# Kernel tuning notes

Measured on AMD Instinct MI355X. Metric: run time of the kernel, lower is better.

## Reference

```python
import jax, jax.numpy as jnp
import numpy as np

B = 64          # batch
N = 256         # input_dim (number of MPS sites / pixels)
BOND = 128      # bond dimension
DF = 2          # feature dimension per pixel
OUT = 10        # output classes
EPS = 1e-12


def _xavier_uniform(key, shape, fan_in, fan_out, gain):
    bound = gain * np.sqrt(6.0 / (fan_in + fan_out))
    return jax.random.uniform(key, shape, jnp.float32, -bound, bound)


def setup_inputs() -> dict:
    key = jax.random.key(0)
    k_x, k_c0, k_cr, k_cl = jax.random.split(key, 4)
    gain = float(np.sqrt(2.0 / (1.0 + 0.01 ** 2)))  # leaky_relu gain
    x = jax.random.uniform(k_x, (B, N), dtype=jnp.float32)  # pixels in [0,1]
    # core 0: (1, DF, BOND); torch fan_in = DF*BOND, fan_out = 1*BOND
    core0 = _xavier_uniform(k_c0, (1, DF, BOND), DF * BOND, BOND, gain)
    # remaining N-1 cores: (BOND, DF, BOND); fan_in = DF*BOND, fan_out = BOND*BOND... torch: fan_in = shape[1]*shape[2] = DF*BOND, fan_out = shape[0]*shape[2] = BOND*BOND? No: fan_out = shape[0]*prod(shape[2:]) = BOND*BOND
    cores = _xavier_uniform(k_cr, (N - 1, BOND, DF, BOND), DF * BOND, BOND * BOND, gain)
    classifier = _xavier_uniform(k_cl, (OUT, BOND), BOND, OUT, gain)
    return {"x": x, "core0": core0, "cores": cores, "classifier": classifier}


def _mps_forward(x, core0, cores, classifier):
    b = x.shape[0]
    H = core0.shape[-1]
    # feature map: pixel v -> (1-v, v)
    feats = jnp.stack([1.0 - x, x], axis=-1)                  # (B, N, DF)
    # contract each core with its pixel feature
    special = jnp.einsum('ldh,bd->blh', core0, feats[:, 0])   # (B, 1, H)
    others = jnp.einsum('nldh,bnd->bnlh', cores, feats[:, 1:])  # (B, N-1, H, H)
    log_norm = jnp.zeros((b,), dtype=x.dtype)

    # log-depth tree contraction; loop bound is static (trace-time)
    while 1 + others.shape[1] > 1:
        # pad the special (1,H) leftmost tensor up to (H,H) with zero rows
        padded = jnp.pad(special, ((0, 0), (0, H - special.shape[1]), (0, 0)))
        full = jnp.concatenate([padded[:, None], others], axis=1)  # (B, K, H, H)
        K = full.shape[1]
        odd = (K % 2 != 0)
        if odd:
            last = full[:, -1]
            full = full[:, :-1]
        s1 = full[:, 0::2]                                    # (B, P, H, H)
        s2 = full[:, 1::2]
        cp = jnp.matmul(s1, s2)                               # (B, P, H, H)
        norms = jnp.maximum(
            jnp.sqrt(jnp.sum(cp * cp, axis=(-2, -1))), EPS)   # (B, P)
        log_norm = log_norm + jnp.sum(jnp.log(norms), axis=1)
        cp = cp / norms[:, :, None, None]
        special = cp[:, 0, 0:1, :]                            # keep only row 0
        others = cp[:, 1:]
        if odd:
            others = jnp.concatenate([others, last[:, None]], axis=1)

    mps_out = special[:, 0, :]                                # (B, H)
    logits = mps_out @ classifier.T + log_norm[:, None]      # (B, OUT)
    return logits


def reference(x, core0, cores, classifier):
    return _mps_forward(x, core0, cores, classifier)
```

## Files before the change

### kernel.cpp

```cpp
#include <hip/hip_runtime.h>
#include <stdint.h>


typedef unsigned short u16;
typedef __attribute__((ext_vector_type(8))) short short8;
typedef __attribute__((ext_vector_type(4))) float f32x4;

#define HP 136

__device__ __forceinline__ u16 f2b(float f) {
  uint32_t u = __builtin_bit_cast(uint32_t, f);
  u += 0x7FFFu + ((u >> 16) & 1u);
  return (u16)(u >> 16);
}
__device__ __forceinline__ float b2f(u16 b) {
  uint32_t u = ((uint32_t)b) << 16;
  return __builtin_bit_cast(float, u);
}

struct AccW { f32x4 t[2][2]; };

__device__ __forceinline__ void mfma_w16(const u16* Alds, const u16* Blds,
                                         AccW& acc) {
  const int tid = threadIdx.x;
  const int wid = tid >> 6, lane = tid & 63;
  const int wm = (wid >> 2) * 32, wn = (wid & 3) * 32;
  const int l16 = lane & 15, quad = lane >> 4;
#pragma unroll
  for (int tm = 0; tm < 2; tm++)
#pragma unroll
    for (int tn = 0; tn < 2; tn++)
      acc.t[tm][tn] = (f32x4){0.f, 0.f, 0.f, 0.f};
#pragma unroll
  for (int kk = 0; kk < 128; kk += 32) {
    short8 af[2], bf[2];
#pragma unroll
    for (int t = 0; t < 2; t++) {
      af[t] = *(const short8*)(Alds + (wm + t * 16 + l16) * HP + kk + quad * 8);
      bf[t] = *(const short8*)(Blds + (wn + t * 16 + l16) * HP + kk + quad * 8);
    }
#pragma unroll
    for (int tm = 0; tm < 2; tm++)
#pragma unroll
      for (int tn = 0; tn < 2; tn++)
        acc.t[tm][tn] = __builtin_amdgcn_mfma_f32_16x16x32_bf16(
            af[tm], bf[tn], acc.t[tm][tn], 0, 0, 0);
  }
}

__device__ __forceinline__ float acc_sumsq(const AccW& acc) {
  float ss = 0.f;
#pragma unroll
  for (int tm = 0; tm < 2; tm++)
#pragma unroll
    for (int tn = 0; tn < 2; tn++)
#pragma unroll
      for (int i = 0; i < 4; i++) {
        float v = acc.t[tm][tn][i];
        ss += v * v;
      }
  return ss;
}

__device__ __forceinline__ void bounce_store(u16* Lb, const AccW& acc, float scale,
                                             bool transposed) {
  const int tid = threadIdx.x;
  const int wid = tid >> 6, lane = tid & 63;
  const int wm = (wid >> 2) * 32, wn = (wid & 3) * 32;
  const int l16 = lane & 15, quad = lane >> 4;
#pragma unroll
  for (int tm = 0; tm < 2; tm++)
#pragma unroll
    for (int tn = 0; tn < 2; tn++)
#pragma unroll
      for (int i = 0; i < 4; i++) {
        int r = wm + tm * 16 + quad * 4 + i;
        int c = wn + tn * 16 + l16;
        int key = transposed ? c : r, sec = transposed ? r : c;
        Lb[key * HP + sec] = f2b(acc.t[tm][tn][i] * scale);
      }
}

__device__ __forceinline__ void copy_out(const u16* Lb, u16* out) {
  const int tid = threadIdx.x;
#pragma unroll
  for (int i = 0; i < 2; i++) {
    int g8 = tid + i * 1024;
    int row = g8 >> 4, c8 = g8 & 15;
    *(uint4*)(out + g8 * 8) = *(const uint4*)(Lb + row * HP + c8 * 8);
  }
}

__device__ __forceinline__ float block_sum(float v, float* red, int nw) {
#pragma unroll
  for (int off = 32; off > 0; off >>= 1) v += __shfl_down(v, off);
  int wid = threadIdx.x >> 6;
  if ((threadIdx.x & 63) == 0) red[wid] = v;
  __syncthreads();
  if (threadIdx.x == 0) {
    float s = 0.f;
    for (int w = 0; w < nw; w++) s += red[w];
    red[0] = s;
  }
  __syncthreads();
  float s = red[0];
  __syncthreads();
  return s;
}

__global__ __launch_bounds__(1024) void k1(const float* __restrict__ cores,
                                           u16* __restrict__ T) {
  __shared__ u16 Ald[128 * HP], B0[128 * HP], B1[128 * HP];
  const int j = blockIdx.x;
  const int p = blockIdx.y;
  const float* c1 = cores + (size_t)(2 * j + 1) * 32768;
  const float* c2 = cores + (size_t)(2 * j + 2) * 32768;
  const int tid = threadIdx.x;
#pragma unroll 4
  for (int i = 0; i < 16; i++) {
    int lh = tid + i * 1024;
    int l = lh >> 7, h = lh & 127;
    float a0 = c1[(l * 2 + 0) * 128 + h];
    float av = p ? (c1[(l * 2 + 1) * 128 + h] - a0) : a0;
    Ald[l * HP + h] = f2b(av);
    float b0 = c2[(l * 2 + 0) * 128 + h];
    float b1 = c2[(l * 2 + 1) * 128 + h];
    B0[h * HP + l] = f2b(b0);
    B1[h * HP + l] = f2b(b1 - b0);
  }
  __syncthreads();
  const bool tr = (j % 2) == 0;
  u16* Tj = T + ((size_t)j * 4 + p * 2) * 16384;
  AccW q0, q1;
  mfma_w16(Ald, B0, q0);
  mfma_w16(Ald, B1, q1);
  __syncthreads();
  bounce_store(Ald, q0, 1.f, tr); __syncthreads();
  copy_out(Ald, Tj + 0 * 16384);  __syncthreads();
  bounce_store(Ald, q1, 1.f, tr); __syncthreads();
  copy_out(Ald, Tj + 1 * 16384);
}

__global__ __launch_bounds__(1024, 8) void k1b(const u16* __restrict__ T,
                                               u16* __restrict__ TT) {
  __shared__ u16 Ald[128 * HP], Bld[128 * HP];
  const int t = blockIdx.x;
  const int j2 = blockIdx.y;
  const int m1 = 2 * j2 + 1, m2 = 2 * j2 + 2;
  const u16* TA = T + ((size_t)m1 * 4 + (t >> 2)) * 16384;
  const u16* TB = T + ((size_t)m2 * 4 + (t & 3)) * 16384;
  const int tid = threadIdx.x;
#pragma unroll
  for (int i = 0; i < 2; i++) {
    int g8 = tid + i * 1024;
    int r = g8 >> 4, c8 = g8 & 15;
    *(uint4*)(Ald + r * HP + c8 * 8) = *(const uint4*)(TA + g8 * 8);
    *(uint4*)(Bld + r * HP + c8 * 8) = *(const uint4*)(TB + g8 * 8);
  }
  __syncthreads();
  AccW acc;
  mfma_w16(Ald, Bld, acc);
  __syncthreads();
  bounce_store(Ald, acc, 1.f, (j2 % 2) == 0);
  __syncthreads();
  copy_out(Ald, TT + ((size_t)j2 * 16 + t) * 16384);
}

__global__ __launch_bounds__(256) void k1c(const u16* __restrict__ TT,
                                           float* __restrict__ Gpart) {
  __shared__ float Gp[1024];
  const int j2 = blockIdx.x, kc = blockIdx.y;
  const int tid = threadIdx.x;
  const int w = tid >> 6, lane = tid & 63;
  const int l16 = lane & 15, quad = lane >> 4;
  const u16* V = TT + (size_t)j2 * 16 * 16384 + (size_t)l16 * 16384;
  const int k0 = kc * 4096 + w * 1024;
  f32x4 acc = (f32x4){0.f, 0.f, 0.f, 0.f};
  for (int kk = k0; kk < k0 + 1024; kk += 32) {
    short8 av = *(const short8*)(V + kk + quad * 8);
    acc = __builtin_amdgcn_mfma_f32_16x16x32_bf16(av, av, acc, 0, 0, 0);
  }
#pragma unroll
  for (int i = 0; i < 4; i++)
    Gp[w * 256 + (quad * 4 + i) * 16 + l16] = acc[i];
  __syncthreads();
  Gpart[((size_t)j2 * 4 + kc) * 256 + tid] =
      Gp[tid] + Gp[256 + tid] + Gp[512 + tid] + Gp[768 + tid];
}

__global__ __launch_bounds__(128) void k2ns(const float* __restrict__ x,
                                            const float* __restrict__ Gpart,
                                            const float* __restrict__ core0,
                                            const float* __restrict__ cores,
                                            const u16* __restrict__ T,
                                            float* __restrict__ cbuf,
                                            float* __restrict__ sA,
                                            float* __restrict__ logs) {
  __shared__ float Gs[256];
  __shared__ float svec[128];
  __shared__ float red[8];
  const int bx = blockIdx.x, tid = threadIdx.x;
  if (bx < 63) {
    const int j2 = bx;
#pragma unroll
    for (int i = 0; i < 2; i++) {
      int t2 = tid + i * 128;
      float s = 0.f;
#pragma unroll
      for (int kc = 0; kc < 4; kc++)
        s += Gpart[((size_t)j2 * 4 + kc) * 256 + t2];
      Gs[t2] = s;
    }
    __syncthreads();
    if (tid < 64) {
      const int b = tid;
      const float* xb = x + b * 256;
      const int m1 = 2 * j2 + 1, m2 = 2 * j2 + 2;
      float a1 = xb[2 * m1 + 2], b1 = xb[2 * m1 + 3];
      float a2 = xb[2 * m2 + 2], b2 = xb[2 * m2 + 3];
      float c1[4] = {1.f, b1, a1, a1 * b1};
      float c2[4] = {1.f, b2, a2, a2 * b2};
      float c[16];
#pragma unroll
      for (int p = 0; p < 4; p++)
#pragma unroll
        for (int q = 0; q < 4; q++) c[p * 4 + q] = c1[p] * c2[q];
      float n2 = 0.f;
#pragma unroll
      for (int t = 0; t < 16; t++) {
        float s = 0.f;
#pragma unroll
        for (int u = 0; u < 16; u++) s += Gs[t * 16 + u] * c[u];
        n2 += c[t] * s;
      }
      float n = fmaxf(sqrtf(n2), 1e-12f);
      logs[b * 127 + 1 + j2] = logf(n);
      float inv = 1.f / n;
#pragma unroll
      for (int t = 0; t < 16; t++)
        cbuf[((size_t)j2 * 64 + b) * 16 + t] = c[t] * inv;
    }
  } else {
    const int b = bx - 63;
    const float* xb = x + b * 256;
    float x0 = xb[0], x1 = xb[1];
    svec[tid] = core0[tid] * (1.f - x0) + core0[128 + tid] * x0;
    __syncthreads();
    float acc1 = 0.f;
    for (int k = 0; k < 128; k++) {
      float m0 = cores[(k * 2 + 0) * 128 + tid];
      float m1 = cores[(k * 2 + 1) * 128 + tid];
      acc1 += svec[k] * (m0 + x1 * (m1 - m0));
    }
    float tot = block_sum(acc1 * acc1, red, 2);
    float n1 = fmaxf(sqrtf(tot), 1e-12f);
    float ln = logf(n1);
    svec[tid] = acc1 / n1;
    __syncthreads();
    float a = xb[2], bb = xb[3], ab = a * bb;
    float acc2 = 0.f;
    for (int k8 = 0; k8 < 16; k8++) {
      union { uint4 v; u16 s[8]; } q00, q01, q10, q11;
      q00.v = *(const uint4*)(T + tid * 128 + k8 * 8);
      q01.v = *(const uint4*)(T + 16384 + tid * 128 + k8 * 8);
      q10.v = *(const uint4*)(T + 32768 + tid * 128 + k8 * 8);
      q11.v = *(const uint4*)(T + 49152 + tid * 128 + k8 * 8);
#pragma unroll
      for (int e = 0; e < 8; e++) {
        float pk = b2f(q00.s[e]) + a * b2f(q10.s[e]) + bb * b2f(q01.s[e]) +
                   ab * b2f(q11.s[e]);
        acc2 += svec[k8 * 8 + e] * pk;
      }
    }
    float tot2 = block_sum(acc2 * acc2, red, 2);
    float n2 = fmaxf(sqrtf(tot2), 1e-12f);
    sA[b * 128 + tid] = acc2 / n2;
    if (tid == 0) logs[b * 127 + 0] = ln + logf(n2);
  }
}

__global__ __launch_bounds__(256, 4) void k2c(const u16* __restrict__ TT,
                                              const float* __restrict__ cbuf,
                                              u16* __restrict__ M0) {
  const int slice = blockIdx.x;
  const int j2 = blockIdx.y;
  const int tid = threadIdx.x;
  const int e0 = slice * 512 + tid * 2;
  float v[16][2];
#pragma unroll
  for (int t = 0; t < 16; t++) {
    union { uint32_t u; u16 s[2]; } q;
    q.u = *(const uint32_t*)(TT + ((size_t)j2 * 16 + t) * 16384 + e0);
    v[t][0] = b2f(q.s[0]);
    v[t][1] = b2f(q.s[1]);
  }
  const float4* cb4 = (const float4*)(cbuf + (size_t)j2 * 1024);
  u16* out = M0 + (size_t)j2 * 16384 + e0;
#pragma unroll 4
  for (int b = 0; b < 64; b++) {
    float4 c0 = cb4[b * 4 + 0];
    float4 c1 = cb4[b * 4 + 1];
    float4 c2 = cb4[b * 4 + 2];
    float4 c3 = cb4[b * 4 + 3];
    float cc[16] = {c0.x, c0.y, c0.z, c0.w, c1.x, c1.y, c1.z, c1.w,
                    c2.x, c2.y, c2.z, c2.w, c3.x, c3.y, c3.z, c3.w};
    float o0 = 0.f, o1 = 0.f;
#pragma unroll
    for (int t = 0; t < 16; t++) {
      o0 += cc[t] * v[t][0];
      o1 += cc[t] * v[t][1];
    }
    union { uint32_t u; u16 s[2]; } r;
    r.s[0] = f2b(o0);
    r.s[1] = f2b(o1);
    *(uint32_t*)(out + (size_t)b * 63 * 16384) = r.u;
  }
}

__global__ __launch_bounds__(1024, 8) void roundk(const u16* __restrict__ In,
                                                  u16* __restrict__ Out,
                                                  const float* __restrict__ sIn,
                                                  float* __restrict__ sOut,
                                                  float* __restrict__ logs,
                                                  int count_in, int slot0) {
  __shared__ u16 Ald[128 * HP], Bld[128 * HP];
  __shared__ float red[16];
  const int b = blockIdx.y, p = blockIdx.x, tid = threadIdx.x;

  if (p == 0) {
    float* svec = (float*)Ald;
    if (tid < 128) svec[tid] = sIn[b * 128 + tid];
    __syncthreads();
    const u16* M = In + (size_t)b * count_in * 16384;
    float acc = 0.f;
    if (tid < 128) {
      for (int k8 = 0; k8 < 16; k8++) {
        union { uint4 v; u16 s[8]; } q;
        q.v = *(const uint4*)(M + tid * 128 + k8 * 8);
#pragma unroll
        for (int e = 0; e < 8; e++) acc += svec[k8 * 8 + e] * b2f(q.s[e]);
      }
    }
    float tot = block_sum((tid < 128) ? acc * acc : 0.f, red, 16);
    float n = fmaxf(sqrtf(tot), 1e-12f);
    if (tid < 128) sOut[b * 128 + tid] = acc / n;
    if (tid == 0) logs[b * 127 + slot0] = logf(n);
  } else {
    const u16* A = In + ((size_t)b * count_in + (2 * p - 1)) * 16384;
    const u16* Bm = In + ((size_t)b * count_in + (2 * p)) * 16384;
#pragma unroll
    for (int i = 0; i < 2; i++) {
      int g8 = tid + i * 1024;
      int r = g8 >> 4, c8 = g8 & 15;
      *(uint4*)(Ald + r * HP + c8 * 8) = *(const uint4*)(A + g8 * 8);
      *(uint4*)(Bld + r * HP + c8 * 8) = *(const uint4*)(Bm + g8 * 8);
    }
    __syncthreads();
    AccW acc;
    mfma_w16(Ald, Bld, acc);
    float tot = block_sum(acc_sumsq(acc), red, 16);
    float n = fmaxf(sqrtf(tot), 1e-12f);
    if (tid == 0) logs[b * 127 + slot0 + p] = logf(n);
    int m = p - 1;
    int count_out = (count_in - 1) / 2;
    bounce_store(Ald, acc, 1.f / n, (m % 2) == 0);
    __syncthreads();
    copy_out(Ald, Out + ((size_t)b * count_out + m) * 16384);
  }
}

__global__ __launch_bounds__(1024, 8) void r7f(const u16* __restrict__ In,
                                               const float* __restrict__ sIn,
                                               const float* __restrict__ logs,
                                               const float* __restrict__ cls,
                                               float* __restrict__ out) {
  __shared__ u16 Ald[128 * HP], Bld[128 * HP];
  __shared__ float svec[128], ovec[128], red[16];
  const int b = blockIdx.x, tid = threadIdx.x;
  if (tid < 128) svec[tid] = sIn[b * 128 + tid];
  const u16* A = In + ((size_t)b * 3 + 1) * 16384;
  const u16* Bm = In + ((size_t)b * 3 + 2) * 16384;
#pragma unroll
  for (int i = 0; i < 2; i++) {
    int g8 = tid + i * 1024;
    int r = g8 >> 4, c8 = g8 & 15;
    *(uint4*)(Ald + r * HP + c8 * 8) = *(const uint4*)(A + g8 * 8);
    *(uint4*)(Bld + r * HP + c8 * 8) = *(const uint4*)(Bm + g8 * 8);
  }
  __syncthreads();
  AccW acc;
  mfma_w16(Ald, Bld, acc);
  float tot = block_sum(acc_sumsq(acc), red, 16);
  float n1 = fmaxf(sqrtf(tot), 1e-12f);
  float lg = logf(n1);
  bounce_store(Ald, acc, 1.f / n1, true);
  const u16* M0p = In + (size_t)b * 3 * 16384;
  float acc0 = 0.f;
  if (tid < 128) {
    for (int k8 = 0; k8 < 16; k8++) {
      union { uint4 v; u16 s[8]; } q;
      q.v = *(const uint4*)(M0p + tid * 128 + k8 * 8);
#pragma unroll
      for (int e = 0; e < 8; e++) acc0 += svec[k8 * 8 + e] * b2f(q.s[e]);
    }
  }
  float tot0 = block_sum((tid < 128) ? acc0 * acc0 : 0.f, red, 16);
  float n0 = fmaxf(sqrtf(tot0), 1e-12f);
  lg += logf(n0);
  if (tid < 128) ovec[tid] = acc0 / n0;
  __syncthreads();
  float acc2 = 0.f;
  if (tid < 128) {
    for (int r = 0; r < 128; r++) acc2 += ovec[r] * b2f(Ald[tid * HP + r]);
  }
  float tot2 = block_sum((tid < 128) ? acc2 * acc2 : 0.f, red, 16);
  float n2 = fmaxf(sqrtf(tot2), 1e-12f);
  lg += logf(n2);
  if (tid < 128) svec[tid] = acc2 / n2;
  __syncthreads();
  if (tid < 10) {
    float a = 0.f;
    for (int h = 0; h < 128; h++) a += svec[h] * cls[tid * 128 + h];
    float L = lg;
    for (int i = 0; i < 124; i++) L += logs[b * 127 + i];
    out[b * 10 + tid] = a + L;
  }
}

extern "C" void kernel_launch(void* const* d_in, const int* in_sizes, int n_in,
                              void* d_out, int out_size, void* d_ws, size_t ws_size,
                              hipStream_t stream) {
  (void)in_sizes; (void)n_in; (void)out_size; (void)ws_size;
  const float* x     = (const float*)d_in[0];
  const float* core0 = (const float*)d_in[1];
  const float* cores = (const float*)d_in[2];
  const float* cls   = (const float*)d_in[3];
  float* out = (float*)d_out;
  char* ws = (char*)d_ws;

  constexpr size_t SZ_T  = (size_t)127 * 4 * 16384 * 2;
  constexpr size_t SZ_A  = (size_t)64 * 31 * 16384 * 2;
  constexpr size_t SZ_M0 = (size_t)64 * 63 * 16384 * 2;

  u16*   T    = (u16*)(ws);
  u16*   TT   = (u16*)(ws + SZ_T);
  u16*   M1   = (u16*)(ws);
  u16*   M0   = (u16*)(ws + SZ_A);
  char*  tail0 = ws + SZ_A + SZ_M0;
  float* Gpart = (float*)(tail0);
  float* cbuf = (float*)(tail0 + 262144);
  float* sA   = (float*)(tail0 + 262144 + 262144);
  float* sB   = (float*)(tail0 + 262144 + 262144 + 32768);
  float* logs = (float*)(tail0 + 262144 + 262144 + 65536);

  k1  <<<dim3(127, 2), 1024, 0, stream>>>(cores, T);
  k1b <<<dim3(16, 63), 1024, 0, stream>>>(T, TT);
  k1c <<<dim3(63, 4), 256, 0, stream>>>(TT, Gpart);
  k2ns<<<dim3(127), 128, 0, stream>>>(x, Gpart, core0, cores, T, cbuf, sA, logs);
  k2c <<<dim3(32, 63), 256, 0, stream>>>(TT, cbuf, M0);
  roundk<<<dim3(32, 64), 1024, 0, stream>>>(M0, M1, sA, sB, logs, 63, 64);
  roundk<<<dim3(16, 64), 1024, 0, stream>>>(M1, M0, sB, sA, logs, 31, 96);
  roundk<<<dim3(8, 64),  1024, 0, stream>>>(M0, M1, sA, sB, logs, 15, 112);
  roundk<<<dim3(4, 64),  1024, 0, stream>>>(M1, M0, sB, sA, logs, 7, 120);
  r7f  <<<dim3(64), 1024, 0, stream>>>(M0, sA, logs, cls, out);
}
```

Before: 261.9 us.

## Fuse pairs of tree-contraction rounds into one kernel and widen k2c vectors

Replaces the four per-round contraction launches with two launches of a fused kernel. Each block multiplies two pairs of matrices, normalises them, and multiplies the results in shared memory, so every other round's intermediate no longer goes through global memory. It also widens k2c to process four elements per thread with half the blocks. The cost is four LDS tiles per block, which lowers occupancy, along with fewer and larger blocks and longer serial work per block.

```diff
diff --git a/kernel.cpp b/kernel.cpp
--- a/kernel.cpp
+++ b/kernel.cpp
@@ -88,6 +88,16 @@
     int g8 = tid + i * 1024;
     int row = g8 >> 4, c8 = g8 & 15;
     *(uint4*)(out + g8 * 8) = *(const uint4*)(Lb + row * HP + c8 * 8);
+  }
+}
+
+__device__ __forceinline__ void loadM(u16* Lb, const u16* __restrict__ src) {
+  const int tid = threadIdx.x;
+#pragma unroll
+  for (int i = 0; i < 2; i++) {
+    int g8 = tid + i * 1024;
+    int r = g8 >> 4, c8 = g8 & 15;
+    *(uint4*)(Lb + r * HP + c8 * 8) = *(const uint4*)(src + g8 * 8);
   }
 }
 
@@ -149,14 +159,8 @@
   const int m1 = 2 * j2 + 1, m2 = 2 * j2 + 2;
   const u16* TA = T + ((size_t)m1 * 4 + (t >> 2)) * 16384;
   const u16* TB = T + ((size_t)m2 * 4 + (t & 3)) * 16384;
-  const int tid = threadIdx.x;
-#pragma unroll
-  for (int i = 0; i < 2; i++) {
-    int g8 = tid + i * 1024;
-    int r = g8 >> 4, c8 = g8 & 15;
-    *(uint4*)(Ald + r * HP + c8 * 8) = *(const uint4*)(TA + g8 * 8);
-    *(uint4*)(Bld + r * HP + c8 * 8) = *(const uint4*)(TB + g8 * 8);
-  }
+  loadM(Ald, TA);
+  loadM(Bld, TB);
   __syncthreads();
   AccW acc;
   mfma_w16(Ald, Bld, acc);
@@ -285,14 +289,14 @@
   const int slice = blockIdx.x;
   const int j2 = blockIdx.y;
   const int tid = threadIdx.x;
-  const int e0 = slice * 512 + tid * 2;
-  float v[16][2];
+  const int e0 = slice * 1024 + tid * 4;
+  float v[16][4];
 #pragma unroll
   for (int t = 0; t < 16; t++) {
-    union { uint32_t u; u16 s[2]; } q;
-    q.u = *(const uint32_t*)(TT + ((size_t)j2 * 16 + t) * 16384 + e0);
-    v[t][0] = b2f(q.s[0]);
-    v[t][1] = b2f(q.s[1]);
+    union { uint2 u; u16 s[4]; } q;
+    q.u = *(const uint2*)(TT + ((size_t)j2 * 16 + t) * 16384 + e0);
+#pragma unroll
+    for (int e = 0; e < 4; e++) v[t][e] = b2f(q.s[e]);
   }
   const float4* cb4 = (const float4*)(cbuf + (size_t)j2 * 1024);
   u16* out = M0 + (size_t)j2 * 16384 + e0;
@@ -304,68 +308,90 @@
     float4 c3 = cb4[b * 4 + 3];
     float cc[16] = {c0.x, c0.y, c0.z, c0.w, c1.x, c1.y, c1.z, c1.w,
                     c2.x, c2.y, c2.z, c2.w, c3.x, c3.y, c3.z, c3.w};
-    float o0 = 0.f, o1 = 0.f;
-#pragma unroll
-    for (int t = 0; t < 16; t++) {
-      o0 += cc[t] * v[t][0];
-      o1 += cc[t] * v[t][1];
-    }
-    union { uint32_t u; u16 s[2]; } r;
-    r.s[0] = f2b(o0);
-    r.s[1] = f2b(o1);
-    *(uint32_t*)(out + (size_t)b * 63 * 16384) = r.u;
-  }
-}
-
-__global__ __launch_bounds__(1024, 8) void roundk(const u16* __restrict__ In,
-                                                  u16* __restrict__ Out,
-                                                  const float* __restrict__ sIn,
-                                                  float* __restrict__ sOut,
-                                                  float* __restrict__ logs,
-                                                  int count_in, int slot0) {
-  __shared__ u16 Ald[128 * HP], Bld[128 * HP];
+    float o[4] = {0.f, 0.f, 0.f, 0.f};
+#pragma unroll
+    for (int t = 0; t < 16; t++)
+#pragma unroll
+      for (int e = 0; e < 4; e++) o[e] += cc[t] * v[t][e];
+    union { uint2 u; u16 s[4]; } r;
+#pragma unroll
+    for (int e = 0; e < 4; e++) r.s[e] = f2b(o[e]);
+    *(uint2*)(out + (size_t)b * 63 * 16384) = r.u;
+  }
+}
+
+__global__ __launch_bounds__(1024, 4) void round2x(const u16* __restrict__ In,
+                                                   u16* __restrict__ Out,
+                                                   const float* __restrict__ sIn,
+                                                   float* __restrict__ sOut,
+                                                   float* __restrict__ logs,
+                                                   int count_in, int count_out,
+                                                   int slot0, int slot1) {
+  __shared__ u16 L0[128 * HP], L1[128 * HP], L2[128 * HP], L3[128 * HP];
   __shared__ float red[16];
   const int b = blockIdx.y, p = blockIdx.x, tid = threadIdx.x;
-
+  const u16* base = In + (size_t)b * count_in * 16384;
   if (p == 0) {
-    float* svec = (float*)Ald;
-    if (tid < 128) svec[tid] = sIn[b * 128 + tid];
-    __syncthreads();
-    const u16* M = In + (size_t)b * count_in * 16384;
-    float acc = 0.f;
+    float* svf = (float*)L3;
+    float* svf2 = svf + 128;
+    if (tid < 128) svf[tid] = sIn[b * 128 + tid];
+    loadM(L0, base + 1 * 16384);
+    loadM(L1, base + 2 * 16384);
+    __syncthreads();
+    float acc0 = 0.f;
     if (tid < 128) {
       for (int k8 = 0; k8 < 16; k8++) {
         union { uint4 v; u16 s[8]; } q;
-        q.v = *(const uint4*)(M + tid * 128 + k8 * 8);
-#pragma unroll
-        for (int e = 0; e < 8; e++) acc += svec[k8 * 8 + e] * b2f(q.s[e]);
+        q.v = *(const uint4*)(base + tid * 128 + k8 * 8);
+#pragma unroll
+        for (int e = 0; e < 8; e++) acc0 += svf[k8 * 8 + e] * b2f(q.s[e]);
       }
     }
-    float tot = block_sum((tid < 128) ? acc * acc : 0.f, red, 16);
-    float n = fmaxf(sqrtf(tot), 1e-12f);
-    if (tid < 128) sOut[b * 128 + tid] = acc / n;
-    if (tid == 0) logs[b * 127 + slot0] = logf(n);
+    float t0 = block_sum((tid < 128) ? acc0 * acc0 : 0.f, red, 16);
+    float n0 = fmaxf(sqrtf(t0), 1e-12f);
+    if (tid == 0) logs[b * 127 + slot0] = logf(n0);
+    if (tid < 128) svf2[tid] = acc0 / n0;
+    AccW acc;
+    mfma_w16(L0, L1, acc);
+    float tq = block_sum(acc_sumsq(acc), red, 16);
+    float nq = fmaxf(sqrtf(tq), 1e-12f);
+    if (tid == 0) logs[b * 127 + slot0 + 1] = logf(nq);
+    bounce_store(L2, acc, 1.f / nq, true);
+    __syncthreads();
+    float acc2 = 0.f;
+    if (tid < 128) {
+      for (int l = 0; l < 128; l++) acc2 += svf2[l] * b2f(L2[tid * HP + l]);
+    }
+    float t2 = block_sum((tid < 128) ? acc2 * acc2 : 0.f, red, 16);
+    float n2 = fmaxf(sqrtf(t2), 1e-12f);
+    if (tid == 0) logs[b * 127 + slot1] = logf(n2);
+    if (tid < 128) sOut[b * 128 + tid] = acc2 / n2;
   } else {
-    const u16* A = In + ((size_t)b * count_in + (2 * p - 1)) * 16384;
-    const u16* Bm = In + ((size_t)b * count_in + (2 * p)) * 16384;
-#pragma unroll
-    for (int i = 0; i < 2; i++) {
-      int g8 = tid + i * 1024;
-      int r = g8 >> 4, c8 = g8 & 15;
-      *(uint4*)(Ald + r * HP + c8 * 8) = *(const uint4*)(A + g8 * 8);
-      *(uint4*)(Bld + r * HP + c8 * 8) = *(const uint4*)(Bm + g8 * 8);
-    }
-    __syncthreads();
+    const int m = p - 1;
+    loadM(L0, base + (size_t)(4 * m + 3) * 16384);
+    loadM(L1, base + (size_t)(4 * m + 4) * 16384);
+    __syncthreads();
+    loadM(L2, base + (size_t)(4 * m + 5) * 16384);
+    loadM(L3, base + (size_t)(4 * m + 6) * 16384);
     AccW acc;
-    mfma_w16(Ald, Bld, acc);
-    float tot = block_sum(acc_sumsq(acc), red, 16);
-    float n = fmaxf(sqrtf(tot), 1e-12f);
-    if (tid == 0) logs[b * 127 + slot0 + p] = logf(n);
-    int m = p - 1;
-    int count_out = (count_in - 1) / 2;
-    bounce_store(Ald, acc, 1.f / n, (m % 2) == 0);
-    __syncthreads();
-    copy_out(Ald, Out + ((size_t)b * count_out + m) * 16384);
+    mfma_w16(L0, L1, acc);
+    float t1 = block_sum(acc_sumsq(acc), red, 16);
+    float n1 = fmaxf(sqrtf(t1), 1e-12f);
+    if (tid == 0) logs[b * 127 + slot0 + 2 + 2 * m] = logf(n1);
+    bounce_store(L0, acc, 1.f / n1, false);
+    mfma_w16(L2, L3, acc);
+    float t2 = block_sum(acc_sumsq(acc), red, 16);
+    float n2 = fmaxf(sqrtf(t2), 1e-12f);
+    if (tid == 0) logs[b * 127 + slot0 + 3 + 2 * m] = logf(n2);
+    bounce_store(L1, acc, 1.f / n2, true);
+    __syncthreads();
+    mfma_w16(L0, L1, acc);
+    float t3 = block_sum(acc_sumsq(acc), red, 16);
+    float n3 = fmaxf(sqrtf(t3), 1e-12f);
+    if (tid == 0) logs[b * 127 + slot1 + 1 + m] = logf(n3);
+    bounce_store(L2, acc, 1.f / n3, (m % 2) == 0);
+    __syncthreads();
+    copy_out(L2, Out + ((size_t)b * count_out + m) * 16384);
   }
 }
 
@@ -380,13 +406,8 @@
   if (tid < 128) svec[tid] = sIn[b * 128 + tid];
   const u16* A = In + ((size_t)b * 3 + 1) * 16384;
   const u16* Bm = In + ((size_t)b * 3 + 2) * 16384;
-#pragma unroll
-  for (int i = 0; i < 2; i++) {
-    int g8 = tid + i * 1024;
-    int r = g8 >> 4, c8 = g8 & 15;
-    *(uint4*)(Ald + r * HP + c8 * 8) = *(const uint4*)(A + g8 * 8);
-    *(uint4*)(Bld + r * HP + c8 * 8) = *(const uint4*)(Bm + g8 * 8);
-  }
+  loadM(Ald, A);
+  loadM(Bld, Bm);
   __syncthreads();
   AccW acc;
   mfma_w16(Ald, Bld, acc);
@@ -444,7 +465,7 @@
 
   u16*   T    = (u16*)(ws);
   u16*   TT   = (u16*)(ws + SZ_T);
-  u16*   M1   = (u16*)(ws);
+  u16*   M2   = (u16*)(ws);
   u16*   M0   = (u16*)(ws + SZ_A);
   char*  tail0 = ws + SZ_A + SZ_M0;
   float* Gpart = (float*)(tail0);
@@ -457,10 +478,8 @@
   k1b <<<dim3(16, 63), 1024, 0, stream>>>(T, TT);
   k1c <<<dim3(63, 4), 256, 0, stream>>>(TT, Gpart);
   k2ns<<<dim3(127), 128, 0, stream>>>(x, Gpart, core0, cores, T, cbuf, sA, logs);
-  k2c <<<dim3(32, 63), 256, 0, stream>>>(TT, cbuf, M0);
-  roundk<<<dim3(32, 64), 1024, 0, stream>>>(M0, M1, sA, sB, logs, 63, 64);
-  roundk<<<dim3(16, 64), 1024, 0, stream>>>(M1, M0, sB, sA, logs, 31, 96);
-  roundk<<<dim3(8, 64),  1024, 0, stream>>>(M0, M1, sA, sB, logs, 15, 112);
-  roundk<<<dim3(4, 64),  1024, 0, stream>>>(M1, M0, sB, sA, logs, 7, 120);
+  k2c <<<dim3(16, 63), 256, 0, stream>>>(TT, cbuf, M0);
+  round2x<<<dim3(16, 64), 1024, 0, stream>>>(M0, M2, sA, sB, logs, 63, 15, 64, 96);
+  round2x<<<dim3(4, 64), 1024, 0, stream>>>(M2, M0, sB, sA, logs, 15, 3, 112, 120);
   r7f  <<<dim3(64), 1024, 0, stream>>>(M0, sA, logs, cls, out);
 }
```

After: 255.0 us. -2.6%, faster.
